# Performance work log

Measured on AMD Instinct MI355X. Metric: run time of the kernel, lower is better.

## Reference

```python
import jax, jax.numpy as jnp
import numpy as np

N, C, H, W = 32, 128, 64, 64
D_BOT, K = 512, 7
EPS = 1e-5


def setup_inputs() -> dict:
    key = jax.random.key(0)
    ks = jax.random.split(key, 4)
    init = lambda k, shape, fan: (jax.random.normal(k, shape, jnp.float32) / np.sqrt(fan).astype(np.float32))
    return {
        "x": jax.random.normal(ks[0], (N, C, H, W), jnp.float32),
        "dw_w": init(ks[1], (C, 1, K, K), K * K),          # depthwise kernel, OIHW with I=1
        "dw_b": jnp.zeros((C,), jnp.float32),
        "gamma": jnp.ones((C,), jnp.float32),
        "beta": jnp.zeros((C,), jnp.float32),
        "pw1_w": init(ks[2], (D_BOT, C), C),               # 1x1 conv == channel matmul
        "pw1_b": jnp.zeros((D_BOT,), jnp.float32),
        "pw2_w": init(ks[3], (C, D_BOT), D_BOT),
        "pw2_b": jnp.zeros((C,), jnp.float32),
    }


def reference(x, dw_w, dw_b, gamma, beta, pw1_w, pw1_b, pw2_w, pw2_b):
    # depthwise 7x7 conv, stride 1, 'same' padding (NCHW)
    y = jax.lax.conv_general_dilated(
        x, dw_w, window_strides=(1, 1), padding="SAME",
        dimension_numbers=("NCHW", "OIHW", "NCHW"),
        feature_group_count=x.shape[1],
    ) + dw_b[None, :, None, None]
    # NCHW -> NHWC for channel LayerNorm
    y = jnp.transpose(y, (0, 2, 3, 1))
    mu = jnp.mean(y, axis=-1, keepdims=True)
    var = jnp.mean(jnp.square(y - mu), axis=-1, keepdims=True)
    y = (y - mu) * jax.lax.rsqrt(var + EPS) * gamma + beta
    # pointwise MLP: 1x1 convs are channel-mixing matmuls
    h = jax.nn.relu(jnp.einsum("nhwc,dc->nhwd", y, pw1_w) + pw1_b)
    o = jnp.einsum("nhwd,cd->nhwc", h, pw2_w) + pw2_b
    # back to NCHW + residual
    return x + jnp.transpose(o, (0, 3, 1, 2))
```

## Files before the change

### kernel.cpp

```cpp
#include <hip/hip_runtime.h>
#include <hip/hip_bf16.h>

#define NB   32
#define CCH  128
#define HH   64
#define WW   64
#define DBOT 512
#define EPS_LN 1e-5f

typedef __attribute__((ext_vector_type(8))) short bf16x8;
typedef __attribute__((ext_vector_type(4))) float f32x4;

__device__ __forceinline__ float bf2f(unsigned short u) {
    return __uint_as_float(((unsigned)u) << 16);
}
__device__ __forceinline__ unsigned short f2bf(float f) {
    __hip_bfloat16 h = __float2bfloat16(f);
    return *(unsigned short*)&h;
}

__global__ __launch_bounds__(256) void wcvt_kernel(
    const float* __restrict__ w1, const float* __restrict__ w2,
    __hip_bfloat16* __restrict__ o1, __hip_bfloat16* __restrict__ o2)
{
    int i = blockIdx.x * 256 + threadIdx.x;
    o1[i] = __float2bfloat16(w1[i]);
    o2[i] = __float2bfloat16(w2[i]);
}

#define XS 76

__global__ __launch_bounds__(256) void dwconv_kernel(
    const float* __restrict__ x, const float* __restrict__ dw_w,
    const float* __restrict__ dw_b, unsigned short* __restrict__ cout)
{
    __shared__ float xs[64 * XS];

    const int t = threadIdx.x;
    const int n = blockIdx.x >> 7;
    const int c = blockIdx.x & 127;

    const float* xp = x + ((size_t)(n * CCH + c) << 12);

    #pragma unroll
    for (int i = 0; i < 4; ++i) {
        int idx = i * 256 + t;
        int r   = idx >> 4;
        int c4  = idx & 15;
        float4 v = ((const float4*)xp)[idx];
        *(float4*)&xs[r * XS + 4 + c4 * 4] = v;
    }
    #pragma unroll
    for (int i = 0; i < 3; ++i) {
        int idx = i * 256 + t;
        int r   = idx / 12;
        int p   = idx % 12;
        int col = (p < 4) ? p : (p + 64);
        xs[r * XS + col] = 0.0f;
    }

    float wgt[49];
    const float* wp = dw_w + c * 49;
    #pragma unroll
    for (int j = 0; j < 49; ++j) wgt[j] = wp[j];
    const float bias = dw_b[c];

    __syncthreads();

    const int h  = t >> 2;
    const int w0 = (t & 3) << 4;

    float acc[16];
    #pragma unroll
    for (int j = 0; j < 16; ++j) acc[j] = bias;

    #pragma unroll
    for (int kh = 0; kh < 7; ++kh) {
        int hh = h + kh - 3;
        if (hh < 0 || hh >= HH) continue;
        float r[24];
        const float* row = &xs[hh * XS + w0];
        #pragma unroll
        for (int j = 0; j < 6; ++j) *(float4*)&r[j * 4] = *(const float4*)&row[j * 4];
        #pragma unroll
        for (int kw = 0; kw < 7; ++kw)
            #pragma unroll
            for (int j = 0; j < 16; ++j)
                acc[j] = fmaf(r[j + kw + 1], wgt[kh * 7 + kw], acc[j]);
    }

    uint4 s0, s1;
    {
        __hip_bfloat162 p0 = __float22bfloat162_rn(make_float2(acc[0],  acc[1]));
        __hip_bfloat162 p1 = __float22bfloat162_rn(make_float2(acc[2],  acc[3]));
        __hip_bfloat162 p2 = __float22bfloat162_rn(make_float2(acc[4],  acc[5]));
        __hip_bfloat162 p3 = __float22bfloat162_rn(make_float2(acc[6],  acc[7]));
        __hip_bfloat162 p4 = __float22bfloat162_rn(make_float2(acc[8],  acc[9]));
        __hip_bfloat162 p5 = __float22bfloat162_rn(make_float2(acc[10], acc[11]));
        __hip_bfloat162 p6 = __float22bfloat162_rn(make_float2(acc[12], acc[13]));
        __hip_bfloat162 p7 = __float22bfloat162_rn(make_float2(acc[14], acc[15]));
        s0.x = *(unsigned*)&p0; s0.y = *(unsigned*)&p1;
        s0.z = *(unsigned*)&p2; s0.w = *(unsigned*)&p3;
        s1.x = *(unsigned*)&p4; s1.y = *(unsigned*)&p5;
        s1.z = *(unsigned*)&p6; s1.w = *(unsigned*)&p7;
    }
    unsigned short* op = cout + ((size_t)((n * 64 + h) * 128 + c) << 6) + w0;
    *(uint4*)op       = s0;
    *(uint4*)(op + 8) = s1;
}

#define HS 136

__global__ __launch_bounds__(256, 4) void mlp_kernel(
    const unsigned short* __restrict__ conv,
    const float* __restrict__ gamma,
    const float* __restrict__ beta,
    const __hip_bfloat16* __restrict__ w1,
    const float* __restrict__ b1,
    const __hip_bfloat16* __restrict__ w2,
    const float* __restrict__ b2,
    const float* __restrict__ x,
    float* __restrict__ out)
{
    __shared__ union {
        unsigned short xs[CCH * 64];
        unsigned short h[64 * HS];
    } u;
    __shared__ float sPart[2][256];
    __shared__ float sMu[64], sRstd[64];

    const int t    = threadIdx.x;
    const int wave = t >> 6;
    const int lane = t & 63;
    const int q    = lane >> 4;
    const int ln   = lane & 15;
    const int wm   = (wave >> 1) * 32;
    const int wn   = (wave & 1) * 64;

    const int n = blockIdx.x >> 6;
    const int h = blockIdx.x & 63;

    {
        const uint4* src = (const uint4*)(conv + ((size_t)blockIdx.x << 13));
        #pragma unroll
        for (int i = 0; i < 4; ++i) {
            int idx = i * 256 + t;
            uint4 v = src[idx];
            *(uint4*)&u.xs[idx * 8] = v;
        }
    }
    __syncthreads();

    {
        const int wI = t & 63, cg = t >> 6;
        float s = 0.f, s2 = 0.f;
        #pragma unroll
        for (int j = 0; j < 32; ++j) {
            float v = bf2f(u.xs[(cg * 32 + j) * 64 + wI]);
            s += v;
            s2 = fmaf(v, v, s2);
        }
        sPart[0][cg * 64 + wI] = s;
        sPart[1][cg * 64 + wI] = s2;
    }
    __syncthreads();
    if (t < 64) {
        float su = 0.f, sq = 0.f;
        #pragma unroll
        for (int g = 0; g < 4; ++g) { su += sPart[0][g * 64 + t]; sq += sPart[1][g * 64 + t]; }
        float mu  = su * (1.0f / 128.0f);
        float var = sq * (1.0f / 128.0f) - mu * mu;
        sMu[t]   = mu;
        sRstd[t] = 1.0f / sqrtf(var + EPS_LN);
    }
    __syncthreads();

    bf16x8 af[2][4];
    #pragma unroll
    for (int mt = 0; mt < 2; ++mt) {
        const int pos = wm + mt * 16 + ln;
        const float mu = sMu[pos], rs = sRstd[pos];
        #pragma unroll
        for (int kb = 0; kb < 4; ++kb) {
            const int c0 = kb * 32 + q * 8;
            float4 g0  = *(const float4*)(gamma + c0);
            float4 g1  = *(const float4*)(gamma + c0 + 4);
            float4 be0 = *(const float4*)(beta + c0);
            float4 be1 = *(const float4*)(beta + c0 + 4);
            float gv[8] = {g0.x, g0.y, g0.z, g0.w, g1.x, g1.y, g1.z, g1.w};
            float bv[8] = {be0.x, be0.y, be0.z, be0.w, be1.x, be1.y, be1.z, be1.w};
            bf16x8 a;
            #pragma unroll
            for (int j = 0; j < 8; ++j) {
                float v = bf2f(u.xs[(c0 + j) * 64 + pos]);
                float r = (v - mu) * rs * gv[j] + bv[j];
                a[j] = (short)f2bf(r);
            }
            af[mt][kb] = a;
        }
    }

    f32x4 oacc[2][4];
    #pragma unroll
    for (int mt = 0; mt < 2; ++mt)
        #pragma unroll
        for (int ct = 0; ct < 4; ++ct) oacc[mt][ct] = (f32x4){0.f, 0.f, 0.f, 0.f};

    for (int dc = 0; dc < 4; ++dc) {
        const int d0 = dc * 128;

        f32x4 hacc[2][4];
        #pragma unroll
        for (int mt = 0; mt < 2; ++mt)
            #pragma unroll
            for (int dt = 0; dt < 4; ++dt) hacc[mt][dt] = (f32x4){0.f, 0.f, 0.f, 0.f};

        #pragma unroll
        for (int kb = 0; kb < 4; ++kb) {
            bf16x8 bw[4];
            #pragma unroll
            for (int dt = 0; dt < 4; ++dt) {
                int d = d0 + wn + dt * 16 + ln;
                bw[dt] = *(const bf16x8*)(w1 + (size_t)d * 128 + kb * 32 + q * 8);
            }
            #pragma unroll
            for (int mt = 0; mt < 2; ++mt)
                #pragma unroll
                for (int dt = 0; dt < 4; ++dt)
                    hacc[mt][dt] = __builtin_amdgcn_mfma_f32_16x16x32_bf16(
                        af[mt][kb], bw[dt], hacc[mt][dt], 0, 0, 0);
        }

        __syncthreads();

        #pragma unroll
        for (int dt = 0; dt < 4; ++dt) {
            const int dl = wn + dt * 16 + ln;
            const float b1v = b1[d0 + dl];
            #pragma unroll
            for (int mt = 0; mt < 2; ++mt) {
                #pragma unroll
                for (int r = 0; r < 4; ++r) {
                    float v = fmaxf(hacc[mt][dt][r] + b1v, 0.0f);
                    u.h[(wm + mt * 16 + q * 4 + r) * HS + dl] = f2bf(v);
                }
            }
        }
        __syncthreads();

        #pragma unroll
        for (int kb = 0; kb < 4; ++kb) {
            bf16x8 ah[2];
            #pragma unroll
            for (int mt = 0; mt < 2; ++mt)
                ah[mt] = *(const bf16x8*)&u.h[(wm + mt * 16 + ln) * HS + kb * 32 + q * 8];
            bf16x8 bw2[4];
            #pragma unroll
            for (int ct = 0; ct < 4; ++ct) {
                int c = wn + ct * 16 + ln;
                bw2[ct] = *(const bf16x8*)(w2 + (size_t)c * DBOT + d0 + kb * 32 + q * 8);
            }
            #pragma unroll
            for (int mt = 0; mt < 2; ++mt)
                #pragma unroll
                for (int ct = 0; ct < 4; ++ct)
                    oacc[mt][ct] = __builtin_amdgcn_mfma_f32_16x16x32_bf16(
                        ah[mt], bw2[ct], oacc[mt][ct], 0, 0, 0);
        }
    }

    #pragma unroll
    for (int ct = 0; ct < 4; ++ct) {
        const int c = wn + ct * 16 + ln;
        const float b2v = b2[c];
        #pragma unroll
        for (int mt = 0; mt < 2; ++mt) {
            size_t base = ((size_t)(n * CCH + c) << 12) + (h << 6) + wm + mt * 16 + q * 4;
            float4 xr = *(const float4*)(x + base);
            float4 o;
            o.x = oacc[mt][ct][0] + b2v + xr.x;
            o.y = oacc[mt][ct][1] + b2v + xr.y;
            o.z = oacc[mt][ct][2] + b2v + xr.z;
            o.w = oacc[mt][ct][3] + b2v + xr.w;
            *(float4*)(out + base) = o;
        }
    }
}

extern "C" void kernel_launch(void* const* d_in, const int* in_sizes, int n_in,
                              void* d_out, int out_size, void* d_ws, size_t ws_size,
                              hipStream_t stream)
{
    const float* x     = (const float*)d_in[0];
    const float* dw_w  = (const float*)d_in[1];
    const float* dw_b  = (const float*)d_in[2];
    const float* gamma = (const float*)d_in[3];
    const float* beta  = (const float*)d_in[4];
    const float* pw1_w = (const float*)d_in[5];
    const float* pw1_b = (const float*)d_in[6];
    const float* pw2_w = (const float*)d_in[7];
    const float* pw2_b = (const float*)d_in[8];
    float* out = (float*)d_out;

    char* ws = (char*)d_ws;
    unsigned short* convb = (unsigned short*)ws;
    __hip_bfloat16* w1b   = (__hip_bfloat16*)(ws + (size_t)33554432);
    __hip_bfloat16* w2b   = (__hip_bfloat16*)(ws + (size_t)33554432 + 131072);

    wcvt_kernel<<<256, 256, 0, stream>>>(pw1_w, pw2_w, w1b, w2b);
    dwconv_kernel<<<NB * CCH, 256, 0, stream>>>(x, dw_w, dw_b, convb);
    mlp_kernel<<<NB * HH, 256, 0, stream>>>(convb, gamma, beta, w1b, pw1_b, w2b, pw2_b, x, out);
}
```

Baseline: 284.7 us.

## Pad dwconv rows, process two image rows per MLP block, pack bf16 conversions

The depthwise conv now zero-pads three halo rows above and below in shared memory, so the inner row loop no longer needs a bounds check and runs fully unrolled. The MLP kernel now uses 512-thread blocks that each handle two image rows with separate shared buffers, halving the grid while doubling shared memory per block. The bf16 conversions and h-tile stores use paired float2-to-bf16x2 packing, and the dc loop is unrolled. Together these aim to cut branch and conversion overhead and improve weight reuse within a CU, at the cost of higher shared-memory and register pressure, which may lower occupancy.

```diff
diff --git a/kernel.cpp b/kernel.cpp
--- a/kernel.cpp
+++ b/kernel.cpp
@@ -30,11 +30,11 @@
 
 #define XS 76
 
-__global__ __launch_bounds__(256) void dwconv_kernel(
+__global__ __launch_bounds__(256, 4) void dwconv_kernel(
     const float* __restrict__ x, const float* __restrict__ dw_w,
     const float* __restrict__ dw_b, unsigned short* __restrict__ cout)
 {
-    __shared__ float xs[64 * XS];
+    __shared__ float xs[70 * XS];
 
     const int t = threadIdx.x;
     const int n = blockIdx.x >> 7;
@@ -48,7 +48,7 @@
         int r   = idx >> 4;
         int c4  = idx & 15;
         float4 v = ((const float4*)xp)[idx];
-        *(float4*)&xs[r * XS + 4 + c4 * 4] = v;
+        *(float4*)&xs[(r + 3) * XS + 4 + c4 * 4] = v;
     }
     #pragma unroll
     for (int i = 0; i < 3; ++i) {
@@ -56,7 +56,16 @@
         int r   = idx / 12;
         int p   = idx % 12;
         int col = (p < 4) ? p : (p + 64);
-        xs[r * XS + col] = 0.0f;
+        xs[(r + 3) * XS + col] = 0.0f;
+    }
+    #pragma unroll
+    for (int i = 0; i < 2; ++i) {
+        int idx = i * 256 + t;
+        if (idx < 456) {
+            int rr = idx / 76, cc = idx % 76;
+            int lr = (rr < 3) ? rr : (rr + 64);
+            xs[lr * XS + cc] = 0.0f;
+        }
     }
 
     float wgt[49];
@@ -76,10 +85,8 @@
 
     #pragma unroll
     for (int kh = 0; kh < 7; ++kh) {
-        int hh = h + kh - 3;
-        if (hh < 0 || hh >= HH) continue;
         float r[24];
-        const float* row = &xs[hh * XS + w0];
+        const float* row = &xs[(h + kh) * XS + w0];
         #pragma unroll
         for (int j = 0; j < 6; ++j) *(float4*)&r[j * 4] = *(const float4*)&row[j * 4];
         #pragma unroll
@@ -111,7 +118,7 @@
 
 #define HS 136
 
-__global__ __launch_bounds__(256, 4) void mlp_kernel(
+__global__ __launch_bounds__(512, 4) void mlp_kernel(
     const unsigned short* __restrict__ conv,
     const float* __restrict__ gamma,
     const float* __restrict__ beta,
@@ -123,55 +130,60 @@
     float* __restrict__ out)
 {
     __shared__ union {
-        unsigned short xs[CCH * 64];
-        unsigned short h[64 * HS];
+        unsigned short xs[2][CCH * 64];
+        unsigned short h[2][64 * HS];
     } u;
-    __shared__ float sPart[2][256];
-    __shared__ float sMu[64], sRstd[64];
-
-    const int t    = threadIdx.x;
-    const int wave = t >> 6;
-    const int lane = t & 63;
-    const int q    = lane >> 4;
-    const int ln   = lane & 15;
-    const int wm   = (wave >> 1) * 32;
-    const int wn   = (wave & 1) * 64;
-
-    const int n = blockIdx.x >> 6;
-    const int h = blockIdx.x & 63;
+    __shared__ float sPart[2][2][256];
+    __shared__ float sMu[2][64], sRstd[2][64];
+
+    const int t     = threadIdx.x;
+    const int rowId = t >> 8;
+    const int tr    = t & 255;
+    const int wave  = tr >> 6;
+    const int lane  = t & 63;
+    const int q     = lane >> 4;
+    const int ln    = lane & 15;
+    const int wm    = (wave >> 1) * 32;
+    const int wn    = (wave & 1) * 64;
+
+    const int grow = blockIdx.x * 2 + rowId;
+    const int n = grow >> 6;
+    const int h = grow & 63;
 
     {
-        const uint4* src = (const uint4*)(conv + ((size_t)blockIdx.x << 13));
+        const uint4* src = (const uint4*)(conv + ((size_t)grow << 13));
         #pragma unroll
         for (int i = 0; i < 4; ++i) {
-            int idx = i * 256 + t;
-            uint4 v = src[idx];
-            *(uint4*)&u.xs[idx * 8] = v;
+            int idx = i * 256 + tr;
+            *(uint4*)&u.xs[rowId][idx * 8] = src[idx];
         }
     }
     __syncthreads();
 
     {
-        const int wI = t & 63, cg = t >> 6;
+        const int wI = tr & 63, cg = tr >> 6;
         float s = 0.f, s2 = 0.f;
         #pragma unroll
         for (int j = 0; j < 32; ++j) {
-            float v = bf2f(u.xs[(cg * 32 + j) * 64 + wI]);
+            float v = bf2f(u.xs[rowId][(cg * 32 + j) * 64 + wI]);
             s += v;
             s2 = fmaf(v, v, s2);
         }
-        sPart[0][cg * 64 + wI] = s;
-        sPart[1][cg * 64 + wI] = s2;
+        sPart[rowId][0][cg * 64 + wI] = s;
+        sPart[rowId][1][cg * 64 + wI] = s2;
     }
     __syncthreads();
-    if (t < 64) {
+    if (tr < 64) {
         float su = 0.f, sq = 0.f;
         #pragma unroll
-        for (int g = 0; g < 4; ++g) { su += sPart[0][g * 64 + t]; sq += sPart[1][g * 64 + t]; }
+        for (int g = 0; g < 4; ++g) {
+            su += sPart[rowId][0][g * 64 + tr];
+            sq += sPart[rowId][1][g * 64 + tr];
+        }
         float mu  = su * (1.0f / 128.0f);
         float var = sq * (1.0f / 128.0f) - mu * mu;
-        sMu[t]   = mu;
-        sRstd[t] = 1.0f / sqrtf(var + EPS_LN);
+        sMu[rowId][tr]   = mu;
+        sRstd[rowId][tr] = 1.0f / sqrtf(var + EPS_LN);
     }
     __syncthreads();
 
@@ -179,7 +191,7 @@
     #pragma unroll
     for (int mt = 0; mt < 2; ++mt) {
         const int pos = wm + mt * 16 + ln;
-        const float mu = sMu[pos], rs = sRstd[pos];
+        const float mu = sMu[rowId][pos], rs = sRstd[rowId][pos];
         #pragma unroll
         for (int kb = 0; kb < 4; ++kb) {
             const int c0 = kb * 32 + q * 8;
@@ -191,10 +203,15 @@
             float bv[8] = {be0.x, be0.y, be0.z, be0.w, be1.x, be1.y, be1.z, be1.w};
             bf16x8 a;
             #pragma unroll
-            for (int j = 0; j < 8; ++j) {
-                float v = bf2f(u.xs[(c0 + j) * 64 + pos]);
-                float r = (v - mu) * rs * gv[j] + bv[j];
-                a[j] = (short)f2bf(r);
+            for (int jp = 0; jp < 4; ++jp) {
+                float v0 = bf2f(u.xs[rowId][(c0 + 2 * jp)     * 64 + pos]);
+                float v1 = bf2f(u.xs[rowId][(c0 + 2 * jp + 1) * 64 + pos]);
+                float r0 = (v0 - mu) * rs * gv[2 * jp]     + bv[2 * jp];
+                float r1 = (v1 - mu) * rs * gv[2 * jp + 1] + bv[2 * jp + 1];
+                __hip_bfloat162 p = __float22bfloat162_rn(make_float2(r0, r1));
+                unsigned pu = *(unsigned*)&p;
+                a[2 * jp]     = (short)(pu & 0xffff);
+                a[2 * jp + 1] = (short)(pu >> 16);
             }
             af[mt][kb] = a;
         }
@@ -206,6 +223,7 @@
         #pragma unroll
         for (int ct = 0; ct < 4; ++ct) oacc[mt][ct] = (f32x4){0.f, 0.f, 0.f, 0.f};
 
+    #pragma unroll
     for (int dc = 0; dc < 4; ++dc) {
         const int d0 = dc * 128;
 
@@ -239,11 +257,18 @@
             const float b1v = b1[d0 + dl];
             #pragma unroll
             for (int mt = 0; mt < 2; ++mt) {
-                #pragma unroll
-                for (int r = 0; r < 4; ++r) {
-                    float v = fmaxf(hacc[mt][dt][r] + b1v, 0.0f);
-                    u.h[(wm + mt * 16 + q * 4 + r) * HS + dl] = f2bf(v);
-                }
+                float v0 = fmaxf(hacc[mt][dt][0] + b1v, 0.0f);
+                float v1 = fmaxf(hacc[mt][dt][1] + b1v, 0.0f);
+                float v2 = fmaxf(hacc[mt][dt][2] + b1v, 0.0f);
+                float v3 = fmaxf(hacc[mt][dt][3] + b1v, 0.0f);
+                __hip_bfloat162 pa = __float22bfloat162_rn(make_float2(v0, v1));
+                __hip_bfloat162 pb = __float22bfloat162_rn(make_float2(v2, v3));
+                unsigned ua = *(unsigned*)&pa, ub = *(unsigned*)&pb;
+                const int rbase = (wm + mt * 16 + q * 4) * HS + dl;
+                u.h[rowId][rbase]          = (unsigned short)(ua & 0xffff);
+                u.h[rowId][rbase + HS]     = (unsigned short)(ua >> 16);
+                u.h[rowId][rbase + 2 * HS] = (unsigned short)(ub & 0xffff);
+                u.h[rowId][rbase + 3 * HS] = (unsigned short)(ub >> 16);
             }
         }
         __syncthreads();
@@ -253,7 +278,7 @@
             bf16x8 ah[2];
             #pragma unroll
             for (int mt = 0; mt < 2; ++mt)
-                ah[mt] = *(const bf16x8*)&u.h[(wm + mt * 16 + ln) * HS + kb * 32 + q * 8];
+                ah[mt] = *(const bf16x8*)&u.h[rowId][(wm + mt * 16 + ln) * HS + kb * 32 + q * 8];
             bf16x8 bw2[4];
             #pragma unroll
             for (int ct = 0; ct < 4; ++ct) {
@@ -309,5 +334,5 @@
 
     wcvt_kernel<<<256, 256, 0, stream>>>(pw1_w, pw2_w, w1b, w2b);
     dwconv_kernel<<<NB * CCH, 256, 0, stream>>>(x, dw_w, dw_b, convb);
-    mlp_kernel<<<NB * HH, 256, 0, stream>>>(convb, gamma, beta, w1b, pw1_b, w2b, pw2_b, x, out);
-}
+    mlp_kernel<<<NB * HH / 2, 512, 0, stream>>>(convb, gamma, beta, w1b, pw1_b, w2b, pw2_b, x, out);
+}
```

Measured after the change: 306.3 us. 1.08x slower.
